# Optimization experiments

Hardware: AMD Instinct MI355X
Metric: run time of the kernel (lower is better)

## Reference

```python
import jax, jax.numpy as jnp
import numpy as np

B, T, C = 4, 2048, 1024
H = 16
D = C // H  # head_dim = 64


def setup_inputs() -> dict:
    key = jax.random.key(0)
    ks = jax.random.split(key, 9)
    s = 1.0 / np.sqrt(C)
    return {
        "x": jax.random.normal(ks[0], (B, T, C), dtype=jnp.float32),
        "Wq": jax.random.normal(ks[1], (C, C), dtype=jnp.float32) * s,
        "bq": jnp.zeros((C,), dtype=jnp.float32),
        "Wk": jax.random.normal(ks[2], (C, C), dtype=jnp.float32) * s,
        "bk": jnp.zeros((C,), dtype=jnp.float32),
        "Wv": jax.random.normal(ks[3], (C, C), dtype=jnp.float32) * s,
        "bv": jnp.zeros((C,), dtype=jnp.float32),
        "Wp": jax.random.normal(ks[4], (C, C), dtype=jnp.float32) * s,
        "bp": jnp.zeros((C,), dtype=jnp.float32),
    }


def reference(x, Wq, bq, Wk, bk, Wv, bv, Wp, bp):
    # Linear projections; reshape to [B, H, T, D]
    def split_heads(y):
        return y.reshape(B, T, H, D).transpose(0, 2, 1, 3)

    q = split_heads(x @ Wq + bq)
    k = split_heads(x @ Wk + bk)
    v = split_heads(x @ Wv + bv)

    scale = 1.0 / np.sqrt(D)
    att = jnp.einsum('bhqd,bhkd->bhqk', q, k) * scale  # [B,H,T,T]
    att = jax.nn.softmax(att, axis=-1)
    # dropout with p=0.0 is identity
    out = jnp.einsum('bhqk,bhkd->bhqd', att, v)        # [B,H,T,D]
    out = out.transpose(0, 2, 1, 3).reshape(B, T, C)
    return out @ Wp + bp
```

## Files before the change

### kernel.cpp

```cpp
#include <hip/hip_runtime.h>


#define B_ 4
#define T_ 2048
#define C_ 1024
#define H_ 16
#define D_ 64

typedef float  f32x4  __attribute__((ext_vector_type(4)));
typedef __bf16 bf16x8 __attribute__((ext_vector_type(8)));
typedef __bf16 bf16x4 __attribute__((ext_vector_type(4)));

typedef const __attribute__((address_space(1))) void gv_t;
typedef __attribute__((address_space(3))) void lds_t;

__device__ __forceinline__ void async_load16(const void* g, void* l) {
  __builtin_amdgcn_global_load_lds((gv_t*)g, (lds_t*)l, 16, 0, 0);
}

__device__ __forceinline__ float fast_exp2(float x) {
#if __has_builtin(__builtin_amdgcn_exp2f)
  return __builtin_amdgcn_exp2f(x);
#else
  return exp2f(x);
#endif
}

__global__ __launch_bounds__(256) void cast_f32_bf16(
    const float* __restrict__ in, __bf16* __restrict__ out, int n) {
  int i = (blockIdx.x * 256 + threadIdx.x) * 8;
  if (i >= n) return;
  float4 a = *(const float4*)(in + i);
  float4 b = *(const float4*)(in + i + 4);
  bf16x8 o;
  o[0] = (__bf16)a.x; o[1] = (__bf16)a.y; o[2] = (__bf16)a.z; o[3] = (__bf16)a.w;
  o[4] = (__bf16)b.x; o[5] = (__bf16)b.y; o[6] = (__bf16)b.z; o[7] = (__bf16)b.w;
  *(bf16x8*)(out + i) = o;
}

__global__ __launch_bounds__(256) void transpose_cast_w(
    const float* __restrict__ W0, const float* __restrict__ W1,
    const float* __restrict__ W2, const float* __restrict__ W3,
    __bf16* __restrict__ out) {
  int z = blockIdx.z;
  const float* W = (z == 0) ? W0 : (z == 1) ? W1 : (z == 2) ? W2 : W3;
  __bf16* o = out + (size_t)z * (C_ * C_);
  __shared__ __align__(16) __bf16 sT[64][72];
  int tid = threadIdx.x;
  int n0 = blockIdx.x * 64, k0 = blockIdx.y * 64;
#pragma unroll
  for (int i = 0; i < 4; i++) {
    int s = tid + i * 256;
    int kr = s >> 4, nc = (s & 15) * 4;
    float4 v = *(const float4*)&W[(size_t)(k0 + kr) * C_ + n0 + nc];
    bf16x4 t;
    t[0] = (__bf16)v.x; t[1] = (__bf16)v.y; t[2] = (__bf16)v.z; t[3] = (__bf16)v.w;
    *(bf16x4*)&sT[kr][nc] = t;
  }
  __syncthreads();
#pragma unroll
  for (int i = 0; i < 2; i++) {
    int s = tid + i * 256;
    int nr = s >> 3, kc = (s & 7) * 8;
    bf16x8 ov;
#pragma unroll
    for (int j = 0; j < 8; j++) ov[j] = sT[kc + j][nr];
    *(bf16x8*)&o[(size_t)(n0 + nr) * C_ + k0 + kc] = ov;
  }
}

template <typename OutT, int EPI>
__device__ __forceinline__ void gemm_body(
    const __bf16* __restrict__ A, const __bf16* __restrict__ Bt,
    const float* __restrict__ bias, OutT* __restrict__ C, int M, int N, int K) {
  __shared__ __align__(16) __bf16 sA[128 * 32];
  __shared__ __align__(16) __bf16 sB[128 * 32];
  int tid = threadIdx.x, lane = tid & 63, wave = tid >> 6;
  int lr = lane & 15, quad = lane >> 4;
  int m0 = blockIdx.y * 128, n0 = blockIdx.x * 128;
  int wm = (wave & 1) * 64, wn = (wave >> 1) * 64;

  const f32x4 zero = {0.f, 0.f, 0.f, 0.f};
  f32x4 acc[4][4];
#pragma unroll
  for (int i = 0; i < 4; i++)
#pragma unroll
    for (int j = 0; j < 4; j++) acc[i][j] = zero;

  for (int k0 = 0; k0 < K; k0 += 32) {
    __syncthreads();
#pragma unroll
    for (int i = 0; i < 2; i++) {
      int s = tid + i * 256;
      int r = s >> 2, c8 = (s & 3) * 8;
      async_load16(A + (size_t)(m0 + r) * K + k0 + c8, &sA[s * 8]);
      async_load16(Bt + (size_t)(n0 + r) * K + k0 + c8, &sB[s * 8]);
    }
    __syncthreads();
    bf16x8 af[4], bfr[4];
#pragma unroll
    for (int mt = 0; mt < 4; mt++)
      af[mt] = *(const bf16x8*)&sA[(wm + mt * 16 + lr) * 32 + quad * 8];
#pragma unroll
    for (int nt = 0; nt < 4; nt++)
      bfr[nt] = *(const bf16x8*)&sB[(wn + nt * 16 + lr) * 32 + quad * 8];
#pragma unroll
    for (int mt = 0; mt < 4; mt++)
#pragma unroll
      for (int nt = 0; nt < 4; nt++)
        acc[mt][nt] = __builtin_amdgcn_mfma_f32_16x16x32_bf16(
            af[mt], bfr[nt], acc[mt][nt], 0, 0, 0);
  }
  if (EPI == 0) {
#pragma unroll
    for (int mt = 0; mt < 4; mt++) {
#pragma unroll
      for (int nt = 0; nt < 4; nt++) {
        int n = n0 + wn + nt * 16 + lr;
        float bv = bias[n];
#pragma unroll
        for (int r = 0; r < 4; r++) {
          int m = m0 + wm + mt * 16 + quad * 4 + r;
          C[(size_t)m * N + n] = (OutT)(acc[mt][nt][r] + bv);
        }
      }
    }
  } else {
    int bb = m0 >> 11;
    int mloc0 = (m0 & (T_ - 1)) + wm;
    __bf16* Ct = (__bf16*)C;
#pragma unroll
    for (int mt = 0; mt < 4; mt++) {
#pragma unroll
      for (int nt = 0; nt < 4; nt++) {
        int n = n0 + wn + nt * 16 + lr;
        float bv = bias[n];
        bf16x4 ov;
#pragma unroll
        for (int r = 0; r < 4; r++) ov[r] = (__bf16)(acc[mt][nt][r] + bv);
        *(bf16x4*)&Ct[((size_t)bb * C_ + n) * T_ + mloc0 + mt * 16 + quad * 4] = ov;
      }
    }
  }
}

__global__ __launch_bounds__(256) void gemm_qkv_kernel(
    const __bf16* __restrict__ A, const __bf16* __restrict__ WT,
    const float* __restrict__ b0, const float* __restrict__ b1,
    const float* __restrict__ b2, __bf16* __restrict__ qkbase,
    __bf16* __restrict__ Vt) {
  int z = blockIdx.z;
  if (z == 2) {
    gemm_body<__bf16, 1>(A, WT + (size_t)2 * C_ * C_, b2, Vt, B_ * T_, C_, C_);
  } else {
    const float* bias = (z == 0) ? b0 : b1;
    gemm_body<__bf16, 0>(A, WT + (size_t)z * C_ * C_, bias,
                         qkbase + (size_t)z * (B_ * T_) * C_, B_ * T_, C_, C_);
  }
}

__global__ __launch_bounds__(256) void gemm_proj_kernel(
    const __bf16* __restrict__ A, const __bf16* __restrict__ Bt,
    const float* __restrict__ bias, float* __restrict__ C) {
  gemm_body<float, 0>(A, Bt, bias, C, B_ * T_, C_, C_);
}

__global__ __launch_bounds__(256) void attn_kernel(
    const __bf16* __restrict__ Q, const __bf16* __restrict__ K,
    const __bf16* __restrict__ Vt, __bf16* __restrict__ O) {
  __shared__ __align__(16) __bf16 sK[64 * 72];
  __shared__ __align__(16) __bf16 sV[64 * 72];
  __shared__ __align__(16) __bf16 sP[4][32 * 72];
  int tid = threadIdx.x, wave = tid >> 6, lane = tid & 63;
  int lr = lane & 15, quad = lane >> 4;
  int bh = blockIdx.y;
  int b = bh >> 4, h = bh & 15;
  int qw = blockIdx.x * 128 + wave * 32;
  __bf16* sPw = &sP[wave][0];

  bf16x8 aq[2][2];
#pragma unroll
  for (int s = 0; s < 2; s++) {
    const __bf16* qp =
        Q + ((size_t)(b * T_ + qw + s * 16 + lr)) * C_ + h * D_ + quad * 8;
    aq[s][0] = *(const bf16x8*)qp;
    aq[s][1] = *(const bf16x8*)(qp + 32);
  }

  bf16x8 onesf;
#pragma unroll
  for (int j = 0; j < 8; j++) onesf[j] = (__bf16)1.0f;

  const f32x4 zero = {0.f, 0.f, 0.f, 0.f};
  f32x4 accO[2][4];
  f32x4 accL[2] = {zero, zero};
#pragma unroll
  for (int s = 0; s < 2; s++)
#pragma unroll
    for (int d = 0; d < 4; d++) accO[s][d] = zero;

  const float cexp = 0.125f * 1.44269504088896340736f;

  int srow[2], sc8[2];
#pragma unroll
  for (int i = 0; i < 2; i++) {
    int s = tid + i * 256;
    srow[i] = s >> 3;
    sc8[i] = (s & 7) * 8;
  }

  bf16x8 kreg[2], vreg[2];
#pragma unroll
  for (int i = 0; i < 2; i++) {
    kreg[i] = *(const bf16x8*)(K + ((size_t)(b * T_ + srow[i])) * C_ + h * D_ + sc8[i]);
    vreg[i] = *(const bf16x8*)(Vt + ((size_t)(bh * D_ + srow[i])) * T_ + sc8[i]);
  }

  for (int k0 = 0; k0 < T_; k0 += 64) {
    __syncthreads();
#pragma unroll
    for (int i = 0; i < 2; i++) {
      *(bf16x8*)&sK[srow[i] * 72 + sc8[i]] = kreg[i];
      *(bf16x8*)&sV[srow[i] * 72 + sc8[i]] = vreg[i];
    }
    __syncthreads();

    if (k0 + 64 < T_) {
      int kn = k0 + 64;
#pragma unroll
      for (int i = 0; i < 2; i++) {
        kreg[i] = *(const bf16x8*)(K + ((size_t)(b * T_ + kn + srow[i])) * C_ + h * D_ + sc8[i]);
        vreg[i] = *(const bf16x8*)(Vt + ((size_t)(bh * D_ + srow[i])) * T_ + kn + sc8[i]);
      }
    }

#pragma unroll
    for (int nt = 0; nt < 4; nt++) {
      bf16x8 bk0 = *(const bf16x8*)&sK[(nt * 16 + lr) * 72 + quad * 8];
      bf16x8 bk1 = *(const bf16x8*)&sK[(nt * 16 + lr) * 72 + 32 + quad * 8];
#pragma unroll
      for (int s = 0; s < 2; s++) {
        f32x4 z = zero;
        z = __builtin_amdgcn_mfma_f32_16x16x32_bf16(bk0, aq[s][0], z, 0, 0, 0);
        z = __builtin_amdgcn_mfma_f32_16x16x32_bf16(bk1, aq[s][1], z, 0, 0, 0);
        bf16x4 pk;
#pragma unroll
        for (int r = 0; r < 4; r++) pk[r] = (__bf16)fast_exp2(z[r] * cexp);
        *(bf16x4*)&sPw[(s * 16 + lr) * 72 + nt * 16 + quad * 4] = pk;
      }
    }

    bf16x8 bp[2][2];
#pragma unroll
    for (int s = 0; s < 2; s++) {
      bp[s][0] = *(const bf16x8*)&sPw[(s * 16 + lr) * 72 + quad * 8];
      bp[s][1] = *(const bf16x8*)&sPw[(s * 16 + lr) * 72 + 32 + quad * 8];
      accL[s] = __builtin_amdgcn_mfma_f32_16x16x32_bf16(onesf, bp[s][0], accL[s], 0, 0, 0);
      accL[s] = __builtin_amdgcn_mfma_f32_16x16x32_bf16(onesf, bp[s][1], accL[s], 0, 0, 0);
    }
#pragma unroll
    for (int dt = 0; dt < 4; dt++) {
      bf16x8 av0 = *(const bf16x8*)&sV[(dt * 16 + lr) * 72 + quad * 8];
      bf16x8 av1 = *(const bf16x8*)&sV[(dt * 16 + lr) * 72 + 32 + quad * 8];
#pragma unroll
      for (int s = 0; s < 2; s++) {
        accO[s][dt] = __builtin_amdgcn_mfma_f32_16x16x32_bf16(av0, bp[s][0], accO[s][dt], 0, 0, 0);
        accO[s][dt] = __builtin_amdgcn_mfma_f32_16x16x32_bf16(av1, bp[s][1], accO[s][dt], 0, 0, 0);
      }
    }
  }

#pragma unroll
  for (int s = 0; s < 2; s++) {
    float inv = 1.0f / accL[s][0];
    __bf16* op =
        O + ((size_t)(b * T_ + qw + s * 16 + lr)) * C_ + h * D_ + quad * 4;
#pragma unroll
    for (int dt = 0; dt < 4; dt++) {
      bf16x4 ov;
#pragma unroll
      for (int r = 0; r < 4; r++) ov[r] = (__bf16)(accO[s][dt][r] * inv);
      *(bf16x4*)&op[dt * 16] = ov;
    }
  }
}

extern "C" void kernel_launch(void* const* d_in, const int* in_sizes, int n_in,
                              void* d_out, int out_size, void* d_ws, size_t ws_size,
                              hipStream_t stream) {
  const float* x  = (const float*)d_in[0];
  const float* Wq = (const float*)d_in[1];
  const float* bq = (const float*)d_in[2];
  const float* Wk = (const float*)d_in[3];
  const float* bk = (const float*)d_in[4];
  const float* Wv = (const float*)d_in[5];
  const float* bv = (const float*)d_in[6];
  const float* Wp = (const float*)d_in[7];
  const float* bp = (const float*)d_in[8];
  float* out = (float*)d_out;

  char* ws = (char*)d_ws;
  const size_t MB = 1024 * 1024;
  __bf16* xb    = (__bf16*)(ws + 0 * MB);
  __bf16* WT    = (__bf16*)(ws + 16 * MB);
  __bf16* Qb    = (__bf16*)(ws + 24 * MB);
  __bf16* Kb    = Qb + (size_t)(B_ * T_) * C_;
  __bf16* Vt    = Kb + (size_t)(B_ * T_) * C_;
  __bf16* attnb = (__bf16*)(ws + 72 * MB);
  __bf16* WpT   = WT + (size_t)3 * C_ * C_;

  cast_f32_bf16<<<dim3(4096), dim3(256), 0, stream>>>(x, xb, B_ * T_ * C_);
  transpose_cast_w<<<dim3(16, 16, 4), dim3(256), 0, stream>>>(Wq, Wk, Wv, Wp, WT);
  gemm_qkv_kernel<<<dim3(8, 64, 3), dim3(256), 0, stream>>>(xb, WT, bq, bk, bv, Qb, Vt);
  attn_kernel<<<dim3(16, 64), dim3(256), 0, stream>>>(Qb, Kb, Vt, attnb);
  gemm_proj_kernel<<<dim3(8, 64), dim3(256), 0, stream>>>(attnb, WpT, bp, out);
}
```

Before: 298.1 us.

## Double-buffer K/V tiles in attention and halve per-wave P scratch

The attention kernel now keeps two LDS buffers for K and V, so the next tile is written while the current one is consumed, dropping one of the two barriers per iteration. Global prefetch moves two tiles ahead. The QK MFMAs for both 16-row sub-tiles are issued first, then P is staged through a single 16-row scratch per wave, reused sequentially for the two sub-tiles. This raises LDS use for K/V and register pressure for the S accumulators, which could lower occupancy.

```diff
diff --git a/kernel.cpp b/kernel.cpp
--- a/kernel.cpp
+++ b/kernel.cpp
@@ -168,9 +168,9 @@
 __global__ __launch_bounds__(256) void attn_kernel(
     const __bf16* __restrict__ Q, const __bf16* __restrict__ K,
     const __bf16* __restrict__ Vt, __bf16* __restrict__ O) {
-  __shared__ __align__(16) __bf16 sK[64 * 72];
-  __shared__ __align__(16) __bf16 sV[64 * 72];
-  __shared__ __align__(16) __bf16 sP[4][32 * 72];
+  __shared__ __align__(16) __bf16 sK[2][64 * 72];
+  __shared__ __align__(16) __bf16 sV[2][64 * 72];
+  __shared__ __align__(16) __bf16 sP[4][16 * 72];
   int tid = threadIdx.x, wave = tid >> 6, lane = tid & 63;
   int lr = lane & 15, quad = lane >> 4;
   int bh = blockIdx.y;
@@ -208,66 +208,100 @@
     srow[i] = s >> 3;
     sc8[i] = (s & 7) * 8;
   }
+  const __bf16* Kb = K + (size_t)b * T_ * C_ + h * D_;
+  const __bf16* Vb = Vt + (size_t)bh * D_ * T_;
 
   bf16x8 kreg[2], vreg[2];
 #pragma unroll
   for (int i = 0; i < 2; i++) {
-    kreg[i] = *(const bf16x8*)(K + ((size_t)(b * T_ + srow[i])) * C_ + h * D_ + sc8[i]);
-    vreg[i] = *(const bf16x8*)(Vt + ((size_t)(bh * D_ + srow[i])) * T_ + sc8[i]);
-  }
-
-  for (int k0 = 0; k0 < T_; k0 += 64) {
+    kreg[i] = *(const bf16x8*)(Kb + (size_t)srow[i] * C_ + sc8[i]);
+    vreg[i] = *(const bf16x8*)(Vb + (size_t)srow[i] * T_ + sc8[i]);
+  }
+#pragma unroll
+  for (int i = 0; i < 2; i++) {
+    *(bf16x8*)&sK[0][srow[i] * 72 + sc8[i]] = kreg[i];
+    *(bf16x8*)&sV[0][srow[i] * 72 + sc8[i]] = vreg[i];
+  }
+#pragma unroll
+  for (int i = 0; i < 2; i++) {
+    kreg[i] = *(const bf16x8*)(Kb + (size_t)(64 + srow[i]) * C_ + sc8[i]);
+    vreg[i] = *(const bf16x8*)(Vb + (size_t)srow[i] * T_ + 64 + sc8[i]);
+  }
+  __syncthreads();
+
+  const int NIT = T_ / 64;
+  for (int it = 0; it < NIT; it++) {
+    const __bf16* cK = &sK[it & 1][0];
+    const __bf16* cV = &sV[it & 1][0];
+    if (it + 1 < NIT) {
+      __bf16* nK = &sK[(it + 1) & 1][0];
+      __bf16* nV = &sV[(it + 1) & 1][0];
+#pragma unroll
+      for (int i = 0; i < 2; i++) {
+        *(bf16x8*)&nK[srow[i] * 72 + sc8[i]] = kreg[i];
+        *(bf16x8*)&nV[srow[i] * 72 + sc8[i]] = vreg[i];
+      }
+    }
+    if (it + 2 < NIT) {
+      int kn = (it + 2) * 64;
+#pragma unroll
+      for (int i = 0; i < 2; i++) {
+        kreg[i] = *(const bf16x8*)(Kb + (size_t)(kn + srow[i]) * C_ + sc8[i]);
+        vreg[i] = *(const bf16x8*)(Vb + (size_t)srow[i] * T_ + kn + sc8[i]);
+      }
+    }
+
+    f32x4 accS0[4], accS1[4];
+#pragma unroll
+    for (int nt = 0; nt < 4; nt++) {
+      bf16x8 bk0 = *(const bf16x8*)&cK[(nt * 16 + lr) * 72 + quad * 8];
+      bf16x8 bk1 = *(const bf16x8*)&cK[(nt * 16 + lr) * 72 + 32 + quad * 8];
+      f32x4 z0 = zero, z1 = zero;
+      z0 = __builtin_amdgcn_mfma_f32_16x16x32_bf16(bk0, aq[0][0], z0, 0, 0, 0);
+      z0 = __builtin_amdgcn_mfma_f32_16x16x32_bf16(bk1, aq[0][1], z0, 0, 0, 0);
+      z1 = __builtin_amdgcn_mfma_f32_16x16x32_bf16(bk0, aq[1][0], z1, 0, 0, 0);
+      z1 = __builtin_amdgcn_mfma_f32_16x16x32_bf16(bk1, aq[1][1], z1, 0, 0, 0);
+      accS0[nt] = z0;
+      accS1[nt] = z1;
+    }
+
+#pragma unroll
+    for (int nt = 0; nt < 4; nt++) {
+      bf16x4 pk;
+#pragma unroll
+      for (int r = 0; r < 4; r++) pk[r] = (__bf16)fast_exp2(accS0[nt][r] * cexp);
+      *(bf16x4*)&sPw[lr * 72 + nt * 16 + quad * 4] = pk;
+    }
+    bf16x8 bp0a = *(const bf16x8*)&sPw[lr * 72 + quad * 8];
+    bf16x8 bp0b = *(const bf16x8*)&sPw[lr * 72 + 32 + quad * 8];
+
+#pragma unroll
+    for (int nt = 0; nt < 4; nt++) {
+      bf16x4 pk;
+#pragma unroll
+      for (int r = 0; r < 4; r++) pk[r] = (__bf16)fast_exp2(accS1[nt][r] * cexp);
+      *(bf16x4*)&sPw[lr * 72 + nt * 16 + quad * 4] = pk;
+    }
+
+    accL[0] = __builtin_amdgcn_mfma_f32_16x16x32_bf16(onesf, bp0a, accL[0], 0, 0, 0);
+    accL[0] = __builtin_amdgcn_mfma_f32_16x16x32_bf16(onesf, bp0b, accL[0], 0, 0, 0);
+
+    bf16x8 bp1a = *(const bf16x8*)&sPw[lr * 72 + quad * 8];
+    bf16x8 bp1b = *(const bf16x8*)&sPw[lr * 72 + 32 + quad * 8];
+    accL[1] = __builtin_amdgcn_mfma_f32_16x16x32_bf16(onesf, bp1a, accL[1], 0, 0, 0);
+    accL[1] = __builtin_amdgcn_mfma_f32_16x16x32_bf16(onesf, bp1b, accL[1], 0, 0, 0);
+
+#pragma unroll
+    for (int dt = 0; dt < 4; dt++) {
+      bf16x8 av0 = *(const bf16x8*)&cV[(dt * 16 + lr) * 72 + quad * 8];
+      bf16x8 av1 = *(const bf16x8*)&cV[(dt * 16 + lr) * 72 + 32 + quad * 8];
+      accO[0][dt] = __builtin_amdgcn_mfma_f32_16x16x32_bf16(av0, bp0a, accO[0][dt], 0, 0, 0);
+      accO[0][dt] = __builtin_amdgcn_mfma_f32_16x16x32_bf16(av1, bp0b, accO[0][dt], 0, 0, 0);
+      accO[1][dt] = __builtin_amdgcn_mfma_f32_16x16x32_bf16(av0, bp1a, accO[1][dt], 0, 0, 0);
+      accO[1][dt] = __builtin_amdgcn_mfma_f32_16x16x32_bf16(av1, bp1b, accO[1][dt], 0, 0, 0);
+    }
+
     __syncthreads();
-#pragma unroll
-    for (int i = 0; i < 2; i++) {
-      *(bf16x8*)&sK[srow[i] * 72 + sc8[i]] = kreg[i];
-      *(bf16x8*)&sV[srow[i] * 72 + sc8[i]] = vreg[i];
-    }
-    __syncthreads();
-
-    if (k0 + 64 < T_) {
-      int kn = k0 + 64;
-#pragma unroll
-      for (int i = 0; i < 2; i++) {
-        kreg[i] = *(const bf16x8*)(K + ((size_t)(b * T_ + kn + srow[i])) * C_ + h * D_ + sc8[i]);
-        vreg[i] = *(const bf16x8*)(Vt + ((size_t)(bh * D_ + srow[i])) * T_ + kn + sc8[i]);
-      }
-    }
-
-#pragma unroll
-    for (int nt = 0; nt < 4; nt++) {
-      bf16x8 bk0 = *(const bf16x8*)&sK[(nt * 16 + lr) * 72 + quad * 8];
-      bf16x8 bk1 = *(const bf16x8*)&sK[(nt * 16 + lr) * 72 + 32 + quad * 8];
-#pragma unroll
-      for (int s = 0; s < 2; s++) {
-        f32x4 z = zero;
-        z = __builtin_amdgcn_mfma_f32_16x16x32_bf16(bk0, aq[s][0], z, 0, 0, 0);
-        z = __builtin_amdgcn_mfma_f32_16x16x32_bf16(bk1, aq[s][1], z, 0, 0, 0);
-        bf16x4 pk;
-#pragma unroll
-        for (int r = 0; r < 4; r++) pk[r] = (__bf16)fast_exp2(z[r] * cexp);
-        *(bf16x4*)&sPw[(s * 16 + lr) * 72 + nt * 16 + quad * 4] = pk;
-      }
-    }
-
-    bf16x8 bp[2][2];
-#pragma unroll
-    for (int s = 0; s < 2; s++) {
-      bp[s][0] = *(const bf16x8*)&sPw[(s * 16 + lr) * 72 + quad * 8];
-      bp[s][1] = *(const bf16x8*)&sPw[(s * 16 + lr) * 72 + 32 + quad * 8];
-      accL[s] = __builtin_amdgcn_mfma_f32_16x16x32_bf16(onesf, bp[s][0], accL[s], 0, 0, 0);
-      accL[s] = __builtin_amdgcn_mfma_f32_16x16x32_bf16(onesf, bp[s][1], accL[s], 0, 0, 0);
-    }
-#pragma unroll
-    for (int dt = 0; dt < 4; dt++) {
-      bf16x8 av0 = *(const bf16x8*)&sV[(dt * 16 + lr) * 72 + quad * 8];
-      bf16x8 av1 = *(const bf16x8*)&sV[(dt * 16 + lr) * 72 + 32 + quad * 8];
-#pragma unroll
-      for (int s = 0; s < 2; s++) {
-        accO[s][dt] = __builtin_amdgcn_mfma_f32_16x16x32_bf16(av0, bp[s][0], accO[s][dt], 0, 0, 0);
-        accO[s][dt] = __builtin_amdgcn_mfma_f32_16x16x32_bf16(av1, bp[s][1], accO[s][dt], 0, 0, 0);
-      }
-    }
   }
 
 #pragma unroll
```

After: 301.1 us. No clear change (+1.0%).
